# Kernel optimization log

Hardware: AMD Instinct MI355X
Metric: run time of the kernel (lower is better)

## Reference

```python
import jax, jax.numpy as jnp
import numpy as np

N_NODES = 100000
N_EDGES = 1600000
IN_CH = 256
OUT_CH = 32
HEADS = 4
NEG_SLOPE = 0.2


def setup_inputs() -> dict:
    key = jax.random.key(0)
    k1, k2, k3, k4, k5 = jax.random.split(key, 5)
    x = jax.random.normal(k1, (N_NODES, IN_CH), dtype=jnp.float32)
    edge_index = jax.random.randint(k2, (2, N_EDGES), 0, N_NODES, dtype=jnp.int64)
    hc = HEADS * OUT_CH
    # glorot init like the torch module
    std_w = np.sqrt(6.0 / (hc + IN_CH))
    W = jax.random.uniform(k3, (hc, IN_CH), dtype=jnp.float32, minval=-std_w, maxval=std_w)
    b = jnp.zeros((hc,), dtype=jnp.float32)
    std_a = np.sqrt(6.0 / (hc + 2))
    att = jax.random.uniform(k4, (hc, 2), dtype=jnp.float32, minval=-std_a, maxval=std_a)
    return {"x": x, "edge_index": edge_index, "W": W, "b": b, "att": att}


def reference(x, edge_index, W, b, att):
    # flow = 'target_to_source': tid=0, sid=1
    tar = edge_index[0]
    src = edge_index[1]
    feat = x @ W.T + b                      # [N, H*C]
    e_pre = feat @ att                      # [N, 2]
    e_src = e_pre[:, 0:1]                   # [N, 1]
    e_tar = e_pre[:, 1:2]                   # [N, 1]
    # edge scores
    e = jnp.exp(jax.nn.leaky_relu(e_src[src] + e_tar[tar], negative_slope=NEG_SLOPE))   # [E, 1]
    e_self = jnp.exp(jax.nn.leaky_relu(e_src + e_tar, negative_slope=NEG_SLOPE))        # [N, 1]
    # softmax denominator over incoming edges + self loop
    e_sum = jax.ops.segment_sum(e, tar, num_segments=N_NODES) + e_self                  # [N, 1]
    alpha_self = e_self / e_sum             # [N, 1]
    alpha = e / e_sum[tar]                  # [E, 1]
    # weighted aggregation (dropout=0 / eval -> identity)
    out = jax.ops.segment_sum(feat[src] * alpha, tar, num_segments=N_NODES)
    out = out + feat * alpha_self           # [N, H*C], concat=True
    return out
```

## Files before the change

kernel.cpp:

```cpp
#include <hip/hip_runtime.h>
#include <hip/hip_bf16.h>
#include <math.h>

#define N_NODES 100000
#define N_EDGES 1600000
#define IN_CH 256
#define HC 128
#define NEG_SLOPE 0.2f

#define NB_C 196
#define CCAP 8704
#define CHUNK 3200

typedef __attribute__((ext_vector_type(8))) short short8;
typedef __attribute__((ext_vector_type(4))) float floatx4;

__device__ inline ushort f2b(float f) {
    __hip_bfloat16 h = __float2bfloat16(f);
    return *(ushort*)&h;
}

__device__ inline float edge_e(float z) {
    float lr = z > 0.f ? z : NEG_SLOPE * z;
    return __expf(lr);
}

#define GBM 128

__global__ __launch_bounds__(256, 2)
void gemm_mfma(const float* __restrict__ x, const float* __restrict__ W,
               const float* __restrict__ b, const float* __restrict__ att,
               __hip_bfloat16* __restrict__ featb,
               float* __restrict__ e_src, float* __restrict__ e_tar,
               float* __restrict__ e_self) {
    __shared__ ushort xs[128][72];
    __shared__ ushort wsh[128][72];

    const int tid  = threadIdx.x;
    const int wave = tid >> 6;
    const int lane = tid & 63;
    const int l16  = lane >> 4;
    const int lc   = lane & 15;
    const int row0 = blockIdx.x * GBM;

    floatx4 acc[2][8];
    #pragma unroll
    for (int mt = 0; mt < 2; ++mt)
        #pragma unroll
        for (int nt = 0; nt < 8; ++nt)
            acc[mt][nt] = (floatx4){0.f, 0.f, 0.f, 0.f};

    for (int kb = 0; kb < 4; ++kb) {
        const int r  = tid >> 4;
        const int kq = tid & 15;
        #pragma unroll
        for (int i = 0; i < 8; ++i) {
            int rr = r + i * 16;
            int gr = row0 + rr;
            float4 v = make_float4(0.f, 0.f, 0.f, 0.f);
            if (gr < N_NODES)
                v = *(const float4*)&x[(size_t)gr * IN_CH + kb * 64 + kq * 4];
            ushort4 u;
            u.x = f2b(v.x); u.y = f2b(v.y); u.z = f2b(v.z); u.w = f2b(v.w);
            *(ushort4*)&xs[rr][kq * 4] = u;
        }
        #pragma unroll
        for (int i = 0; i < 8; ++i) {
            int rr = r + i * 16;
            float4 v = *(const float4*)&W[(size_t)rr * IN_CH + kb * 64 + kq * 4];
            ushort4 u;
            u.x = f2b(v.x); u.y = f2b(v.y); u.z = f2b(v.z); u.w = f2b(v.w);
            *(ushort4*)&wsh[rr][kq * 4] = u;
        }
        __syncthreads();
        #pragma unroll
        for (int ks = 0; ks < 2; ++ks) {
            short8 a0 = *(short8*)&xs[wave * 32 + lc][ks * 32 + l16 * 8];
            short8 a1 = *(short8*)&xs[wave * 32 + 16 + lc][ks * 32 + l16 * 8];
            short8 bf[8];
            #pragma unroll
            for (int nt = 0; nt < 8; ++nt)
                bf[nt] = *(short8*)&wsh[nt * 16 + lc][ks * 32 + l16 * 8];
            #pragma unroll
            for (int nt = 0; nt < 8; ++nt) {
                acc[0][nt] = __builtin_amdgcn_mfma_f32_16x16x32_bf16(a0, bf[nt], acc[0][nt], 0, 0, 0);
                acc[1][nt] = __builtin_amdgcn_mfma_f32_16x16x32_bf16(a1, bf[nt], acc[1][nt], 0, 0, 0);
            }
        }
        __syncthreads();
    }

    float av0[8], av1[8], bc[8];
    #pragma unroll
    for (int nt = 0; nt < 8; ++nt) {
        float2 av = *(const float2*)&att[(nt * 16 + lc) * 2];
        av0[nt] = av.x; av1[nt] = av.y;
        bc[nt] = b[nt * 16 + lc];
    }

    #pragma unroll
    for (int mt = 0; mt < 2; ++mt) {
        #pragma unroll
        for (int rg = 0; rg < 4; ++rg) {
            int row = row0 + wave * 32 + mt * 16 + l16 * 4 + rg;
            float s = 0.f, t = 0.f;
            float vals[8];
            #pragma unroll
            for (int nt = 0; nt < 8; ++nt) {
                float v = acc[mt][nt][rg] + bc[nt];
                vals[nt] = v;
                s += v * av0[nt];
                t += v * av1[nt];
            }
            #pragma unroll
            for (int off = 8; off; off >>= 1) {
                s += __shfl_xor(s, off);
                t += __shfl_xor(t, off);
            }
            if (row < N_NODES) {
                if (lc == 0) {
                    e_src[row] = s;
                    e_tar[row] = t;
                    float z = s + t;
                    float lr = z > 0.f ? z : NEG_SLOPE * z;
                    e_self[row] = __expf(lr);
                }
                #pragma unroll
                for (int nt = 0; nt < 8; ++nt)
                    featb[(size_t)row * HC + nt * 16 + lc] = __float2bfloat16(vals[nt]);
            }
        }
    }
}

__global__ __launch_bounds__(256)
void bin2_k(const int* __restrict__ ei, int* __restrict__ gcur,
            int* __restrict__ ebuf) {
    __shared__ int lcnt[NB_C];
    __shared__ int lcur[NB_C];
    const int base = blockIdx.x * CHUNK;

    for (int i = threadIdx.x; i < NB_C; i += 256) lcnt[i] = 0;
    __syncthreads();

    for (int i = threadIdx.x; i < CHUNK; i += 256)
        atomicAdd(&lcnt[ei[base + i] >> 9], 1);
    __syncthreads();

    for (int bkt = threadIdx.x; bkt < NB_C; bkt += 256) {
        int c = lcnt[bkt];
        lcur[bkt] = c ? atomicAdd(&gcur[bkt], c) : 0;
    }
    __syncthreads();

    for (int i = threadIdx.x; i < CHUNK; i += 256) {
        int t = ei[base + i];
        int s = ei[N_EDGES + base + i];
        int bkt = t >> 9;
        int pos = atomicAdd(&lcur[bkt], 1);
        if (pos < CCAP)
            ebuf[bkt * CCAP + pos] = s | ((t & 511) << 17);
    }
}

__global__ __launch_bounds__(512)
void bucket_csr2_k(const int* __restrict__ gcur, const int* __restrict__ ebuf,
                   const float* __restrict__ e_src, const float* __restrict__ e_tar,
                   int* __restrict__ offsets, int* __restrict__ csr_src,
                   float* __restrict__ ewb) {
    const int b = blockIdx.x;
    const int tid = threadIdx.x;

    __shared__ int sc[256];
    __shared__ int lcnt[512];
    __shared__ int lofs[512];
    __shared__ int lout[CCAP];
    __shared__ float ltar[512];

    {
        int n = b * 512 + tid;
        ltar[tid] = (n < N_NODES) ? e_tar[n] : 0.f;
    }

    if (tid < 256) {
        int c = 0;
        if (tid < NB_C) { c = gcur[tid]; if (c > CCAP) c = CCAP; }
        sc[tid] = c;
    }
    lcnt[tid] = 0;
    __syncthreads();
    #pragma unroll
    for (int off = 1; off < 256; off <<= 1) {
        int v = 0;
        if (tid < 256) v = sc[tid] + ((tid >= off) ? sc[tid - off] : 0);
        __syncthreads();
        if (tid < 256) sc[tid] = v;
        __syncthreads();
    }
    int count = gcur[b]; if (count > CCAP) count = CCAP;
    const int base = (b == 0) ? 0 : sc[b - 1];

    const int* st = &ebuf[b * CCAP];
    for (int i = tid; i < count; i += 512)
        atomicAdd(&lcnt[st[i] >> 17], 1);
    __syncthreads();

    lofs[tid] = lcnt[tid];
    __syncthreads();
    for (int off = 1; off < 512; off <<= 1) {
        int v = lofs[tid] + ((tid >= off) ? lofs[tid - off] : 0);
        __syncthreads();
        lofs[tid] = v;
        __syncthreads();
    }
    int excl = lofs[tid] - lcnt[tid];
    lcnt[tid] = excl;

    {
        int n0 = b * 512 + tid;
        if (n0 < N_NODES) offsets[n0] = base + excl;
    }
    if (b == NB_C - 1 && tid == 0) offsets[N_NODES] = base + count;
    __syncthreads();

    for (int i = tid; i < count; i += 512) {
        int v = st[i];
        int pos = atomicAdd(&lcnt[v >> 17], 1);
        lout[pos] = v;
    }
    __syncthreads();

    for (int i = tid; i < count; i += 512) {
        int v = lout[i];
        int src = v & 0x1FFFF;
        csr_src[base + i] = src;
        ewb[base + i] = edge_e(e_src[src] + ltar[v >> 17]);
    }
}

__global__ __launch_bounds__(256)
void aggregate_k(const int* __restrict__ offsets, const int* __restrict__ csr_src,
                 const float* __restrict__ ewb,
                 const __hip_bfloat162* __restrict__ featb,
                 const float* __restrict__ e_self, float* __restrict__ out) {
    int node = blockIdx.x * 4 + (threadIdx.x >> 6);
    if (node >= N_NODES) return;
    int lane = threadIdx.x & 63;
    int beg = offsets[node];
    int end = offsets[node + 1];
    float eself = e_self[node];

    float2 fs = __bfloat1622float2(featb[(size_t)node * 64 + lane]);
    float esum = eself;
    float accx = eself * fs.x, accy = eself * fs.y;

    int j = beg;
    int npeel = (4 - (j & 3)) & 3;
    if (npeel > end - j) npeel = end - j;
    for (int p = 0; p < npeel; ++p, ++j) {
        int s0 = csr_src[j];
        float e0 = ewb[j];
        float2 f0 = __bfloat1622float2(featb[(size_t)s0 * 64 + lane]);
        esum += e0; accx += e0 * f0.x; accy += e0 * f0.y;
    }

    for (; j + 7 < end; j += 8) {
        int4 a = *(const int4*)&csr_src[j];
        int4 c = *(const int4*)&csr_src[j + 4];
        float4 eA = *(const float4*)&ewb[j];
        float4 eB = *(const float4*)&ewb[j + 4];
        float2 f0 = __bfloat1622float2(featb[(size_t)a.x * 64 + lane]);
        float2 f1 = __bfloat1622float2(featb[(size_t)a.y * 64 + lane]);
        float2 f2 = __bfloat1622float2(featb[(size_t)a.z * 64 + lane]);
        float2 f3 = __bfloat1622float2(featb[(size_t)a.w * 64 + lane]);
        float2 f4 = __bfloat1622float2(featb[(size_t)c.x * 64 + lane]);
        float2 f5 = __bfloat1622float2(featb[(size_t)c.y * 64 + lane]);
        float2 f6 = __bfloat1622float2(featb[(size_t)c.z * 64 + lane]);
        float2 f7 = __bfloat1622float2(featb[(size_t)c.w * 64 + lane]);
        esum += ((eA.x + eA.y) + (eA.z + eA.w)) + ((eB.x + eB.y) + (eB.z + eB.w));
        accx += eA.x * f0.x + eA.y * f1.x + eA.z * f2.x + eA.w * f3.x;
        accx += eB.x * f4.x + eB.y * f5.x + eB.z * f6.x + eB.w * f7.x;
        accy += eA.x * f0.y + eA.y * f1.y + eA.z * f2.y + eA.w * f3.y;
        accy += eB.x * f4.y + eB.y * f5.y + eB.z * f6.y + eB.w * f7.y;
    }
    for (; j + 3 < end; j += 4) {
        int4 a = *(const int4*)&csr_src[j];
        float4 eA = *(const float4*)&ewb[j];
        float2 f0 = __bfloat1622float2(featb[(size_t)a.x * 64 + lane]);
        float2 f1 = __bfloat1622float2(featb[(size_t)a.y * 64 + lane]);
        float2 f2 = __bfloat1622float2(featb[(size_t)a.z * 64 + lane]);
        float2 f3 = __bfloat1622float2(featb[(size_t)a.w * 64 + lane]);
        esum += (eA.x + eA.y) + (eA.z + eA.w);
        accx += eA.x * f0.x + eA.y * f1.x + eA.z * f2.x + eA.w * f3.x;
        accy += eA.x * f0.y + eA.y * f1.y + eA.z * f2.y + eA.w * f3.y;
    }
    for (; j < end; ++j) {
        int s0 = csr_src[j];
        float e0 = ewb[j];
        float2 f0 = __bfloat1622float2(featb[(size_t)s0 * 64 + lane]);
        esum += e0;
        accx += e0 * f0.x;
        accy += e0 * f0.y;
    }
    float inv = 1.f / esum;
    *(float2*)&out[(size_t)node * HC + lane * 2] = make_float2(accx * inv, accy * inv);
}

extern "C" void kernel_launch(void* const* d_in, const int* in_sizes, int n_in,
                              void* d_out, int out_size, void* d_ws, size_t ws_size,
                              hipStream_t stream) {
    const float* x   = (const float*)d_in[0];
    const int*   ei  = (const int*)d_in[1];
    const float* W   = (const float*)d_in[2];
    const float* b   = (const float*)d_in[3];
    const float* att = (const float*)d_in[4];
    float* out = (float*)d_out;

    unsigned char* p = (unsigned char*)d_ws;
    auto take = [&](size_t bytes) {
        unsigned char* r = p;
        p += (bytes + 255) & ~(size_t)255;
        return (void*)r;
    };
    __hip_bfloat16* featb = (__hip_bfloat16*)take((size_t)N_NODES * HC * sizeof(__hip_bfloat16));
    float* e_src   = (float*)take((size_t)N_NODES * sizeof(float));
    float* e_tar   = (float*)take((size_t)N_NODES * sizeof(float));
    float* e_self  = (float*)take((size_t)N_NODES * sizeof(float));
    int*   offsets = (int*)take((size_t)(N_NODES + 1) * sizeof(int));
    int*   gcur    = (int*)take((size_t)NB_C * sizeof(int));
    int*   csr_src = (int*)take((size_t)N_EDGES * sizeof(int));
    float* ewb     = (float*)take((size_t)N_EDGES * sizeof(float));
    int*   ebuf    = (int*)take((size_t)NB_C * CCAP * sizeof(int));

    (void)hipMemsetAsync(gcur, 0, NB_C * sizeof(int), stream);

    gemm_mfma<<<(N_NODES + GBM - 1) / GBM, 256, 0, stream>>>(x, W, b, att, featb,
                                                             e_src, e_tar, e_self);

    bin2_k<<<N_EDGES / CHUNK, 256, 0, stream>>>(ei, gcur, ebuf);
    bucket_csr2_k<<<NB_C, 512, 0, stream>>>(gcur, ebuf, e_src, e_tar,
                                            offsets, csr_src, ewb);

    aggregate_k<<<(N_NODES + 3) / 4, 256, 0, stream>>>(offsets, csr_src, ewb,
                                                       (const __hip_bfloat162*)featb,
                                                       e_self, out);
}
```

Before: 306.0 us.

## Split aggregation wave into four edge groups with 16-byte row loads; preconvert W

```diff
diff --git a/kernel.cpp b/kernel.cpp
--- a/kernel.cpp
+++ b/kernel.cpp
@@ -25,10 +25,22 @@
     return __expf(lr);
 }
 
+__device__ inline float bflo(unsigned u) { return __uint_as_float(u << 16); }
+__device__ inline float bfhi(unsigned u) { return __uint_as_float(u & 0xffff0000u); }
+
+__global__ __launch_bounds__(256)
+void wconv_k(const float* __restrict__ W, ushort* __restrict__ wb) {
+    int i = blockIdx.x * 256 + threadIdx.x;
+    float4 v = *(const float4*)&W[(size_t)i * 4];
+    ushort4 u;
+    u.x = f2b(v.x); u.y = f2b(v.y); u.z = f2b(v.z); u.w = f2b(v.w);
+    *(ushort4*)&wb[(size_t)i * 4] = u;
+}
+
 #define GBM 128
 
 __global__ __launch_bounds__(256, 2)
-void gemm_mfma(const float* __restrict__ x, const float* __restrict__ W,
+void gemm_mfma(const float* __restrict__ x, const ushort* __restrict__ wb,
                const float* __restrict__ b, const float* __restrict__ att,
                __hip_bfloat16* __restrict__ featb,
                float* __restrict__ e_src, float* __restrict__ e_tar,
@@ -67,10 +79,8 @@
         #pragma unroll
         for (int i = 0; i < 8; ++i) {
             int rr = r + i * 16;
-            float4 v = *(const float4*)&W[(size_t)rr * IN_CH + kb * 64 + kq * 4];
-            ushort4 u;
-            u.x = f2b(v.x); u.y = f2b(v.y); u.z = f2b(v.z); u.w = f2b(v.w);
-            *(ushort4*)&wsh[rr][kq * 4] = u;
+            *(ushort4*)&wsh[rr][kq * 4] =
+                *(const ushort4*)&wb[(size_t)rr * IN_CH + kb * 64 + kq * 4];
         }
         __syncthreads();
         #pragma unroll
@@ -241,69 +251,91 @@
 __global__ __launch_bounds__(256)
 void aggregate_k(const int* __restrict__ offsets, const int* __restrict__ csr_src,
                  const float* __restrict__ ewb,
-                 const __hip_bfloat162* __restrict__ featb,
+                 const __hip_bfloat16* __restrict__ featb,
                  const float* __restrict__ e_self, float* __restrict__ out) {
     int node = blockIdx.x * 4 + (threadIdx.x >> 6);
     if (node >= N_NODES) return;
     int lane = threadIdx.x & 63;
+    int g = lane >> 4;
+    int q = lane & 15;
     int beg = offsets[node];
     int end = offsets[node + 1];
     float eself = e_self[node];
 
-    float2 fs = __bfloat1622float2(featb[(size_t)node * 64 + lane]);
-    float esum = eself;
-    float accx = eself * fs.x, accy = eself * fs.y;
+    const char* fb = (const char*)featb;
+    const size_t qofs = (size_t)(q * 16);
+
+    uint4 su = *(const uint4*)(fb + (size_t)node * 256 + qofs);
+    float m0 = (g == 0) ? eself : 0.f;
+    float esum = m0;
+    float acc[8];
+    acc[0] = m0 * bflo(su.x); acc[1] = m0 * bfhi(su.x);
+    acc[2] = m0 * bflo(su.y); acc[3] = m0 * bfhi(su.y);
+    acc[4] = m0 * bflo(su.z); acc[5] = m0 * bfhi(su.z);
+    acc[6] = m0 * bflo(su.w); acc[7] = m0 * bfhi(su.w);
 
     int j = beg;
-    int npeel = (4 - (j & 3)) & 3;
-    if (npeel > end - j) npeel = end - j;
-    for (int p = 0; p < npeel; ++p, ++j) {
-        int s0 = csr_src[j];
-        float e0 = ewb[j];
-        float2 f0 = __bfloat1622float2(featb[(size_t)s0 * 64 + lane]);
-        esum += e0; accx += e0 * f0.x; accy += e0 * f0.y;
-    }
-
     for (; j + 7 < end; j += 8) {
-        int4 a = *(const int4*)&csr_src[j];
-        int4 c = *(const int4*)&csr_src[j + 4];
-        float4 eA = *(const float4*)&ewb[j];
-        float4 eB = *(const float4*)&ewb[j + 4];
-        float2 f0 = __bfloat1622float2(featb[(size_t)a.x * 64 + lane]);
-        float2 f1 = __bfloat1622float2(featb[(size_t)a.y * 64 + lane]);
-        float2 f2 = __bfloat1622float2(featb[(size_t)a.z * 64 + lane]);
-        float2 f3 = __bfloat1622float2(featb[(size_t)a.w * 64 + lane]);
-        float2 f4 = __bfloat1622float2(featb[(size_t)c.x * 64 + lane]);
-        float2 f5 = __bfloat1622float2(featb[(size_t)c.y * 64 + lane]);
-        float2 f6 = __bfloat1622float2(featb[(size_t)c.z * 64 + lane]);
-        float2 f7 = __bfloat1622float2(featb[(size_t)c.w * 64 + lane]);
-        esum += ((eA.x + eA.y) + (eA.z + eA.w)) + ((eB.x + eB.y) + (eB.z + eB.w));
-        accx += eA.x * f0.x + eA.y * f1.x + eA.z * f2.x + eA.w * f3.x;
-        accx += eB.x * f4.x + eB.y * f5.x + eB.z * f6.x + eB.w * f7.x;
-        accy += eA.x * f0.y + eA.y * f1.y + eA.z * f2.y + eA.w * f3.y;
-        accy += eB.x * f4.y + eB.y * f5.y + eB.z * f6.y + eB.w * f7.y;
+        int s0 = csr_src[j + g];
+        int s1 = csr_src[j + 4 + g];
+        float e0 = ewb[j + g];
+        float e1 = ewb[j + 4 + g];
+        uint4 u0 = *(const uint4*)(fb + (size_t)s0 * 256 + qofs);
+        uint4 u1 = *(const uint4*)(fb + (size_t)s1 * 256 + qofs);
+        esum += e0 + e1;
+        acc[0] += e0 * bflo(u0.x) + e1 * bflo(u1.x);
+        acc[1] += e0 * bfhi(u0.x) + e1 * bfhi(u1.x);
+        acc[2] += e0 * bflo(u0.y) + e1 * bflo(u1.y);
+        acc[3] += e0 * bfhi(u0.y) + e1 * bfhi(u1.y);
+        acc[4] += e0 * bflo(u0.z) + e1 * bflo(u1.z);
+        acc[5] += e0 * bfhi(u0.z) + e1 * bfhi(u1.z);
+        acc[6] += e0 * bflo(u0.w) + e1 * bflo(u1.w);
+        acc[7] += e0 * bfhi(u0.w) + e1 * bfhi(u1.w);
     }
     for (; j + 3 < end; j += 4) {
-        int4 a = *(const int4*)&csr_src[j];
-        float4 eA = *(const float4*)&ewb[j];
-        float2 f0 = __bfloat1622float2(featb[(size_t)a.x * 64 + lane]);
-        float2 f1 = __bfloat1622float2(featb[(size_t)a.y * 64 + lane]);
-        float2 f2 = __bfloat1622float2(featb[(size_t)a.z * 64 + lane]);
-        float2 f3 = __bfloat1622float2(featb[(size_t)a.w * 64 + lane]);
-        esum += (eA.x + eA.y) + (eA.z + eA.w);
-        accx += eA.x * f0.x + eA.y * f1.x + eA.z * f2.x + eA.w * f3.x;
-        accy += eA.x * f0.y + eA.y * f1.y + eA.z * f2.y + eA.w * f3.y;
+        int s0 = csr_src[j + g];
+        float e0 = ewb[j + g];
+        uint4 u0 = *(const uint4*)(fb + (size_t)s0 * 256 + qofs);
+        esum += e0;
+        acc[0] += e0 * bflo(u0.x);
+        acc[1] += e0 * bfhi(u0.x);
+        acc[2] += e0 * bflo(u0.y);
+        acc[3] += e0 * bfhi(u0.y);
+        acc[4] += e0 * bflo(u0.z);
+        acc[5] += e0 * bfhi(u0.z);
+        acc[6] += e0 * bflo(u0.w);
+        acc[7] += e0 * bfhi(u0.w);
     }
     for (; j < end; ++j) {
         int s0 = csr_src[j];
-        float e0 = ewb[j];
-        float2 f0 = __bfloat1622float2(featb[(size_t)s0 * 64 + lane]);
-        esum += e0;
-        accx += e0 * f0.x;
-        accy += e0 * f0.y;
-    }
-    float inv = 1.f / esum;
-    *(float2*)&out[(size_t)node * HC + lane * 2] = make_float2(accx * inv, accy * inv);
+        float ew = ewb[j];
+        uint4 u0 = *(const uint4*)(fb + (size_t)s0 * 256 + qofs);
+        float em = (g == 0) ? ew : 0.f;
+        esum += em;
+        acc[0] += em * bflo(u0.x);
+        acc[1] += em * bfhi(u0.x);
+        acc[2] += em * bflo(u0.y);
+        acc[3] += em * bfhi(u0.y);
+        acc[4] += em * bflo(u0.z);
+        acc[5] += em * bfhi(u0.z);
+        acc[6] += em * bflo(u0.w);
+        acc[7] += em * bfhi(u0.w);
+    }
+
+    #pragma unroll
+    for (int k = 0; k < 8; ++k) {
+        acc[k] += __shfl_xor(acc[k], 16);
+        acc[k] += __shfl_xor(acc[k], 32);
+    }
+    esum += __shfl_xor(esum, 16);
+    esum += __shfl_xor(esum, 32);
+
+    if (g == 0) {
+        float inv = 1.f / esum;
+        float* op = &out[(size_t)node * HC + q * 8];
+        *(float4*)op = make_float4(acc[0] * inv, acc[1] * inv, acc[2] * inv, acc[3] * inv);
+        *(float4*)(op + 4) = make_float4(acc[4] * inv, acc[5] * inv, acc[6] * inv, acc[7] * inv);
+    }
 }
 
 extern "C" void kernel_launch(void* const* d_in, const int* in_sizes, int n_in,
@@ -331,10 +363,12 @@
     int*   csr_src = (int*)take((size_t)N_EDGES * sizeof(int));
     float* ewb     = (float*)take((size_t)N_EDGES * sizeof(float));
     int*   ebuf    = (int*)take((size_t)NB_C * CCAP * sizeof(int));
+    ushort* wb     = (ushort*)take((size_t)HC * IN_CH * sizeof(ushort));
 
     (void)hipMemsetAsync(gcur, 0, NB_C * sizeof(int), stream);
 
-    gemm_mfma<<<(N_NODES + GBM - 1) / GBM, 256, 0, stream>>>(x, W, b, att, featb,
+    wconv_k<<<(HC * IN_CH) / (256 * 4), 256, 0, stream>>>(W, wb);
+    gemm_mfma<<<(N_NODES + GBM - 1) / GBM, 256, 0, stream>>>(x, wb, b, att, featb,
                                                              e_src, e_tar, e_self);
 
     bin2_k<<<N_EDGES / CHUNK, 256, 0, stream>>>(ei, gcur, ebuf);
@@ -342,6 +376,5 @@
                                             offsets, csr_src, ewb);
 
     aggregate_k<<<(N_NODES + 3) / 4, 256, 0, stream>>>(offsets, csr_src, ewb,
-                                                       (const __hip_bfloat162*)featb,
-                                                       e_self, out);
-}
+                                                       featb, e_self, out);
+}
```

After: 302.1 us. About the same (-1.3%).
